# Kernel optimization log

Measured on AMD Instinct MI355X. Metric: run time of the kernel, lower is better.

## Reference

```python
import jax, jax.numpy as jnp
import numpy as np

B, T, R, D = 32, 128, 49, 512
H_EXP, H_CLS = 256, 256
THRES = 0.1
LAM = 4.0
NEG_INF = -1e9


def setup_inputs() -> dict:
    key = jax.random.key(0)
    ks = jax.random.split(key, 16)
    s = 0.02
    return {
        "word_emb": jax.random.normal(ks[0], (B, T, D), jnp.float32),
        "region_emb": jax.random.normal(ks[1], (B, R, D), jnp.float32),
        "attention_mask": jnp.ones((B, T), jnp.int32),
        # pos expert MLP: D -> H_EXP -> 1
        "pw1": jax.random.normal(ks[2], (D, H_EXP), jnp.float32) * s,
        "pb1": jnp.zeros((H_EXP,), jnp.float32),
        "pw2": jax.random.normal(ks[3], (H_EXP, 1), jnp.float32) * s,
        "pb2": jnp.zeros((1,), jnp.float32),
        # neg expert MLP: D -> H_EXP -> 1
        "nw1": jax.random.normal(ks[4], (D, H_EXP), jnp.float32) * s,
        "nb1": jnp.zeros((H_EXP,), jnp.float32),
        "nw2": jax.random.normal(ks[5], (H_EXP, 1), jnp.float32) * s,
        "nb2": jnp.zeros((1,), jnp.float32),
        # fc: D -> 1
        "fcw": jax.random.normal(ks[6], (D, 1), jnp.float32) * s,
        "fcb": jnp.zeros((1,), jnp.float32),
        # classifier: D -> H_CLS -> 2 (dropout is eval-mode identity)
        "cw1": jax.random.normal(ks[7], (D, H_CLS), jnp.float32) * s,
        "cb1": jnp.zeros((H_CLS,), jnp.float32),
        "cw2": jax.random.normal(ks[8], (H_CLS, 2), jnp.float32) * s,
        "cb2": jnp.zeros((2,), jnp.float32),
    }


def _mlp_score(x, w1, b1, w2, b2):
    # sigmoid(Linear(tanh(Linear(x)))) -> squeeze last dim
    return jax.nn.sigmoid(jnp.tanh(x @ w1 + b1) @ w2 + b2)[..., 0]


def reference(word_emb, region_emb, attention_mask,
              pw1, pb1, pw2, pb2, nw1, nb1, nw2, nb2,
              fcw, fcb, cw1, cb1, cw2, cb2):
    mask_f = attention_mask.astype(word_emb.dtype)  # [B,T]

    # cross attention word x region: [B,T,R]
    attn = jnp.einsum("btd,brd->btr", word_emb, region_emb)
    attn_neg = (attn - THRES > 0).astype(attn.dtype)  # [B,T,R]
    attn_pos = jax.nn.softmax(
        jnp.where(attn_neg > 0, attn, NEG_INF) * LAM, axis=-1)
    pos = jnp.einsum("btr,brd->btd", attn_pos, region_emb) + word_emb

    # pos expert: sigmoid score, zeroed where token has no positive region
    # or is padding (padding tokens were excluded by the ragged gather).
    expert_neg_mask = attn_neg.sum(-1) == 0  # [B,T] bool
    pos_score = _mlp_score(pos, pw1, pb1, pw2, pb2)  # [B,T]
    pos_score = jnp.where(expert_neg_mask, 0.0, pos_score) * mask_f
    pos_score = jax.nn.relu(pos_score)
    pos_agg = jnp.einsum("bt,btd->bd", pos_score, pos)

    # neg expert over all (token, region) pair embeddings, masked to the
    # ragged set neg_mask = (1 - attn_neg) * attention_mask
    all_emb = word_emb[:, :, None, :] + region_emb[:, None, :, :]  # [B,T,R,D]
    neg_mask = (1.0 - attn_neg) * mask_f[:, :, None]  # [B,T,R]
    neg_score = _mlp_score(all_emb, nw1, nb1, nw2, nb2)  # [B,T,R]
    neg_score = jax.nn.relu(neg_score * neg_mask)
    neg_agg = jnp.einsum("btr,btrd->bd", neg_score, all_emb)

    result = jnp.stack([neg_agg, pos_agg], axis=1)  # [B,2,D]

    choose = (result @ fcw + fcb)[..., 0]  # [B,2]
    choose_mask = attn_neg.sum(axis=(-1, -2)) == 0  # [B]
    choose = choose.at[:, 0].set(
        jnp.where(choose_mask, NEG_INF, choose[:, 0]))
    path_prob = jax.nn.softmax(choose, axis=-1)  # [B,2]
    final = jnp.einsum("bk,bkd->bd", path_prob, result)  # [B,D]

    logits = jax.nn.relu(final @ cw1 + cb1) @ cw2 + cb2  # [B,2]
    return (logits, path_prob)
```

## Files before the change

kernel.cpp:

```cpp
#include <hip/hip_runtime.h>

#define B_ 32
#define T_ 128
#define R_ 49
#define D_ 512
#define HE_ 256
#define HC_ 256

#define NG_PACK 64
#define NG_K1 512
#define NG_G1 354
#define NG_G2 256
#define NG_NEGB 512

typedef float f32x4 __attribute__((ext_vector_type(4)));
typedef short s16x8 __attribute__((ext_vector_type(8)));
typedef short s16x4 __attribute__((ext_vector_type(4)));

__device__ __forceinline__ unsigned short bf16rne(float f) {
  unsigned u = __float_as_uint(f);
  u += 0x7FFF + ((u >> 16) & 1);
  return (unsigned short)(u >> 16);
}
__device__ __forceinline__ float rcp_fast(float x) {
  return __builtin_amdgcn_rcpf(x);
}
__device__ __forceinline__ float tanh_fast(float x) {
  float e = __expf(2.0f * x);
  return fmaf(-2.0f, rcp_fast(e + 1.0f), 1.0f);
}
__device__ __forceinline__ float sigmoid_fast(float x) {
  return rcp_fast(1.0f + __expf(-x));
}
__device__ __forceinline__ float wave_sum(float v) {
#pragma unroll
  for (int off = 32; off; off >>= 1) v += __shfl_down(v, off);
  return v;
}

__global__ __launch_bounds__(512, 8) void k1_pack(
    const float* __restrict__ word, const float* __restrict__ region,
    const float* __restrict__ nw1, const float* __restrict__ pw1,
    const int* __restrict__ amask, unsigned short* __restrict__ wp,
    float* __restrict__ nsr, float* __restrict__ pos,
    float* __restrict__ negcnt, unsigned long long* __restrict__ nmask) {
  __shared__ float attn_s[8][52];
  __shared__ alignas(16) float wp_T[49][8];
  int tid = threadIdx.x, wave = tid >> 6, lane = tid & 63;
  int bid = blockIdx.x;

  if (bid < NG_PACK) {
    int gid = bid * 512 + tid;
    if (gid < B_ * R_) nsr[gid] = 0.f;
    int mat = gid >> 14;
    int rem = gid & 16383;
    int plane = rem & 63;
    int tile = rem >> 6;
    int kt = tile >> 4, ct = tile & 15;
    const float* W = mat ? pw1 : nw1;
    int k0 = kt * 32 + (plane >> 4) * 8;
    int c = ct * 16 + (plane & 15);
    s16x8 pk;
#pragma unroll
    for (int j = 0; j < 8; ++j)
      pk[j] = (short)bf16rne(W[(size_t)(k0 + j) * HE_ + c]);
    *(s16x8*)(wp + (size_t)gid * 8) = pk;
    return;
  }

  int bid2 = bid - NG_PACK;
  int b = bid2 >> 4;
  int t0 = (bid2 & 15) * 8;
  int bt0 = b * T_ + t0;
  const float* reg = region + (size_t)b * R_ * D_;
  const float4* word4 = (const float4*)word;

#pragma unroll
  for (int pass = 0; pass < 2; ++pass) {
    int tp = pass * 4;
    float4 wv[4][2];
#pragma unroll
    for (int t = 0; t < 4; ++t)
#pragma unroll
      for (int j = 0; j < 2; ++j)
        wv[t][j] = word4[(size_t)(bt0 + tp + t) * 128 + lane * 2 + j];
    for (int r = wave; r < R_; r += 8) {
      const float4* rrow4 = (const float4*)(reg + (size_t)r * D_);
      float4 rv0 = rrow4[lane * 2 + 0];
      float4 rv1 = rrow4[lane * 2 + 1];
#pragma unroll
      for (int t = 0; t < 4; ++t) {
        float4 w0 = wv[t][0], w1 = wv[t][1];
        float acc = 0.f;
        acc = fmaf(w0.x, rv0.x, acc);
        acc = fmaf(w0.y, rv0.y, acc);
        acc = fmaf(w0.z, rv0.z, acc);
        acc = fmaf(w0.w, rv0.w, acc);
        acc = fmaf(w1.x, rv1.x, acc);
        acc = fmaf(w1.y, rv1.y, acc);
        acc = fmaf(w1.z, rv1.z, acc);
        acc = fmaf(w1.w, rv1.w, acc);
        acc = wave_sum(acc);
        if (lane == 0) attn_s[tp + t][r] = acc;
      }
    }
  }
  __syncthreads();

  {
    int t = wave;
    int am = amask[bt0 + t];
    float a = (lane < R_) ? attn_s[t][lane] : 0.f;
    float neg = (lane < R_ && (a - 0.1f) > 0.f) ? 1.f : 0.f;
    float masked = (lane < R_) ? ((neg > 0.f) ? a * 4.0f : -4e9f) : -3.0e38f;
    float cnt = wave_sum(neg);
    float m = masked;
#pragma unroll
    for (int off = 32; off; off >>= 1) m = fmaxf(m, __shfl_down(m, off));
    m = __shfl(m, 0);
    float e = (lane < R_) ? __expf(masked - m) : 0.f;
    float s = wave_sum(e);
    s = __shfl(s, 0);
    if (lane < R_) wp_T[lane][t] = e / s;
    bool want = (lane < R_) && (neg == 0.f) && (am != 0);
    unsigned long long bm = __ballot(want);
    if (lane == 0) {
      negcnt[bt0 + t] = cnt;
      nmask[bt0 + t] = bm;
    }
  }
  __syncthreads();

  int d = tid;
  float accs[8] = {0.f, 0.f, 0.f, 0.f, 0.f, 0.f, 0.f, 0.f};
#pragma unroll 7
  for (int r = 0; r < R_; ++r) {
    float g = reg[(size_t)r * D_ + d];
    float4 w0 = *(const float4*)&wp_T[r][0];
    float4 w1 = *(const float4*)&wp_T[r][4];
    accs[0] = fmaf(w0.x, g, accs[0]);
    accs[1] = fmaf(w0.y, g, accs[1]);
    accs[2] = fmaf(w0.z, g, accs[2]);
    accs[3] = fmaf(w0.w, g, accs[3]);
    accs[4] = fmaf(w1.x, g, accs[4]);
    accs[5] = fmaf(w1.y, g, accs[5]);
    accs[6] = fmaf(w1.z, g, accs[6]);
    accs[7] = fmaf(w1.w, g, accs[7]);
  }
#pragma unroll
  for (int t = 0; t < 8; ++t) {
    size_t base = (size_t)(bt0 + t) * D_ + d;
    pos[base] = word[base] + accs[t];
  }
}

__global__ __launch_bounds__(512) void gemm_all(
    const float* __restrict__ word, const float* __restrict__ region,
    const float* __restrict__ pos, const unsigned short* __restrict__ wpack,
    const float* __restrict__ nb1, const float* __restrict__ pb1,
    const float* __restrict__ pw2, const float* __restrict__ pb2,
    const float* __restrict__ negcnt, const int* __restrict__ amask,
    float* __restrict__ wh, float* __restrict__ rh,
    float* __restrict__ pscore) {
  __shared__ alignas(16) unsigned short As[16 * 512];
  __shared__ float sred[16][4];
  int tid = threadIdx.x, wave = tid >> 6, lane = tid & 63;
  int bid = blockIdx.x;

  bool isg2 = (bid >= NG_G1);
  const float* A;
  float* outp = nullptr;
  int row0;
  bool useb = false;
  const s16x8* Wp8;
  if (!isg2) {
    if (bid < 256) {
      A = word; outp = wh; row0 = bid * 16; useb = true;
    } else {
      A = region; outp = rh; row0 = (bid - 256) * 16;
    }
    Wp8 = (const s16x8*)wpack;
  } else {
    A = pos; row0 = (bid - NG_G1) * 16;
    Wp8 = (const s16x8*)wpack + 16384;
  }
  const float4* A4 = (const float4*)(A + (size_t)row0 * D_);
#pragma unroll
  for (int it = 0; it < 4; ++it) {
    int f = it * 512 + tid;
    int row = f >> 7, kq = f & 127;
    float4 v = A4[f];
    int bo = (row * 1024 + kq * 8) ^ ((row & 7) << 4);
    s16x4 pk;
    pk[0] = (short)bf16rne(v.x);
    pk[1] = (short)bf16rne(v.y);
    pk[2] = (short)bf16rne(v.z);
    pk[3] = (short)bf16rne(v.w);
    *(s16x4*)((char*)As + bo) = pk;
  }
  __syncthreads();
  int rl = lane & 15, kg = lane >> 4;
  f32x4 acc0 = {0.f, 0.f, 0.f, 0.f}, acc1 = {0.f, 0.f, 0.f, 0.f};
  int ct0 = wave, ct1 = wave + 8;
#pragma unroll
  for (int kt = 0; kt < 16; ++kt) {
    int bo = (rl * 1024 + kt * 64 + kg * 16) ^ ((rl & 7) << 4);
    s16x8 af = *(const s16x8*)((char*)As + bo);
    s16x8 b0 = Wp8[(size_t)(kt * 16 + ct0) * 64 + lane];
    s16x8 b1 = Wp8[(size_t)(kt * 16 + ct1) * 64 + lane];
    acc0 = __builtin_amdgcn_mfma_f32_16x16x32_bf16(af, b0, acc0, 0, 0, 0);
    acc1 = __builtin_amdgcn_mfma_f32_16x16x32_bf16(af, b1, acc1, 0, 0, 0);
  }
  if (!isg2) {
    float bb0 = useb ? nb1[ct0 * 16 + rl] : 0.f;
    float bb1 = useb ? nb1[ct1 * 16 + rl] : 0.f;
    int r0 = row0 + kg * 4;
#pragma unroll
    for (int q = 0; q < 4; ++q) {
      outp[(size_t)(r0 + q) * HE_ + ct0 * 16 + rl] = acc0[q] + bb0;
      outp[(size_t)(r0 + q) * HE_ + ct1 * 16 + rl] = acc1[q] + bb1;
    }
    return;
  }
  __syncthreads();
  float* hp_s = (float*)As;
#pragma unroll
  for (int q = 0; q < 4; ++q) {
    hp_s[(kg * 4 + q) * 256 + ct0 * 16 + rl] = acc0[q];
    hp_s[(kg * 4 + q) * 256 + ct1 * 16 + rl] = acc1[q];
  }
  __syncthreads();
  int c = tid & 255, jh = tid >> 8;
  float pb1c = pb1[c], pw2c = pw2[c];
#pragma unroll
  for (int jj = 0; jj < 8; ++jj) {
    int j = jh * 8 + jj;
    float v = tanh_fast(hp_s[j * 256 + c] + pb1c) * pw2c;
    v = wave_sum(v);
    if (lane == 0) sred[j][wave & 3] = v;
  }
  __syncthreads();
  if (tid < 16) {
    float s = sred[tid][0] + sred[tid][1] + sred[tid][2] + sred[tid][3] +
              pb2[0];
    s = sigmoid_fast(s);
    int row = row0 + tid;
    if (negcnt[row] == 0.f) s = 0.f;
    s *= (float)amask[row];
    pscore[row] = fmaxf(s, 0.f);
  }
}

__global__ __launch_bounds__(512, 6) void neg_expert(
    const float* __restrict__ wh, const float* __restrict__ rh,
    const float* __restrict__ nw2, const float* __restrict__ nb2,
    const unsigned long long* __restrict__ nmask, float* __restrict__ nst,
    float* __restrict__ nsr) {
  __shared__ alignas(16) float rh_s[R_ * HE_];
  __shared__ int plist[400];
  __shared__ float nst_l[8];
  __shared__ float nsr_l[52];
  __shared__ int cnt_s[8];
  __shared__ int off_s[8];
  __shared__ int P_s;
  int tid = threadIdx.x, wave = tid >> 6, lane = tid & 63;
  int nb = blockIdx.x;
  int b = nb >> 4, t0 = (nb & 15) * 8;
  int bt0 = b * T_ + t0;
  {
    const float4* src = (const float4*)(rh + (size_t)b * R_ * HE_);
    float4* dst = (float4*)rh_s;
    for (int i = tid; i < R_ * (HE_ / 4); i += 512) dst[i] = src[i];
  }
  if (tid < 8) {
    nst_l[tid] = 0.f;
    cnt_s[tid] = __popcll(nmask[bt0 + tid]);
  }
  if (tid < R_) nsr_l[tid] = 0.f;
  __syncthreads();
  if (tid == 0) {
    int tot = 0;
#pragma unroll
    for (int w = 0; w < 8; ++w) {
      off_s[w] = tot;
      tot += cnt_s[w];
    }
    P_s = tot;
  }
  __syncthreads();
  {
    unsigned long long mw = nmask[bt0 + wave];
    if (lane < R_ && ((mw >> lane) & 1ull)) {
      int pfx = __popcll(mw & ((1ull << lane) - 1ull));
      plist[off_s[wave] + pfx] = (wave << 6) | lane;
    }
  }
  __syncthreads();
  int P = P_s;
  int grp = tid >> 4, gl = tid & 15;
  float4 wnr[4];
#pragma unroll
  for (int k = 0; k < 4; ++k)
    wnr[k] = ((const float4*)nw2)[4 * gl + ((gl + k) & 3)];
  float bias = nb2[0];
  for (int i = grp; i < P; i += 32) {
    int tr = plist[i];
    int t = tr >> 6, r = tr & 63;
    const float4* wrow = (const float4*)(wh + (size_t)(bt0 + t) * HE_);
    const float4* rrow = (const float4*)(rh_s + r * HE_);
    float acc = 0.f;
#pragma unroll
    for (int k = 0; k < 4; ++k) {
      int c = 4 * gl + ((gl + k) & 3);
      float4 hw = wrow[c];
      float4 hr = rrow[c];
      float4 wn = wnr[k];
      acc = fmaf(tanh_fast(hw.x + hr.x), wn.x, acc);
      acc = fmaf(tanh_fast(hw.y + hr.y), wn.y, acc);
      acc = fmaf(tanh_fast(hw.z + hr.z), wn.z, acc);
      acc = fmaf(tanh_fast(hw.w + hr.w), wn.w, acc);
    }
    acc += __shfl_xor(acc, 1);
    acc += __shfl_xor(acc, 2);
    acc += __shfl_xor(acc, 4);
    acc += __shfl_xor(acc, 8);
    if (gl == 0) {
      float s = sigmoid_fast(acc + bias);
      atomicAdd(&nst_l[t], s);
      atomicAdd(&nsr_l[r], s);
    }
  }
  __syncthreads();
  if (tid < 8) {
    nst[bt0 + tid] = nst_l[tid];
  } else if (tid >= 64 && tid < 64 + R_) {
    atomicAdd(&nsr[b * R_ + (tid - 64)], nsr_l[tid - 64]);
  }
}

__global__ __launch_bounds__(512) void k7a_agg(
    const float* __restrict__ word, const float* __restrict__ region,
    const float* __restrict__ pos, const float* __restrict__ pscore,
    const float* __restrict__ nst, const float* __restrict__ nsr,
    float* __restrict__ nagg, float* __restrict__ pagg) {
  int b = blockIdx.x >> 3, dc = blockIdx.x & 7;
  int tid = threadIdx.x;
  int dl = tid & 63, ts = tid >> 6;
  int d = dc * 64 + dl;
  __shared__ float nst_s[T_], psc_s[T_], nsr_s[R_];
  __shared__ float redn[8][64], redp[8][64];
  if (tid < T_) {
    psc_s[tid] = pscore[b * T_ + tid];
    nst_s[tid] = nst[b * T_ + tid];
  } else if (tid < T_ + R_) {
    nsr_s[tid - T_] = nsr[b * R_ + (tid - T_)];
  }
  __syncthreads();
  float na = 0.f, pa = 0.f;
  for (int t = ts; t < T_; t += 8) {
    size_t base = ((size_t)(b * T_ + t)) * D_ + d;
    na = fmaf(nst_s[t], word[base], na);
    pa = fmaf(psc_s[t], pos[base], pa);
  }
  for (int r = ts; r < R_; r += 8)
    na = fmaf(nsr_s[r], region[((size_t)(b * R_ + r)) * D_ + d], na);
  redn[ts][dl] = na;
  redp[ts][dl] = pa;
  __syncthreads();
  if (tid < 64) {
    float s = 0.f;
#pragma unroll
    for (int k = 0; k < 8; ++k) s += redn[k][tid];
    nagg[(size_t)b * D_ + dc * 64 + tid] = s;
  } else if (tid < 128) {
    int l = tid - 64;
    float s = 0.f;
#pragma unroll
    for (int k = 0; k < 8; ++k) s += redp[k][l];
    pagg[(size_t)b * D_ + dc * 64 + l] = s;
  }
}

__global__ __launch_bounds__(256) void k7b_tail(
    const float* __restrict__ nagg, const float* __restrict__ pagg,
    const float* __restrict__ negcnt, const float* __restrict__ fcw,
    const float* __restrict__ fcb, const float* __restrict__ cw1,
    const float* __restrict__ cb1, const float* __restrict__ cw2,
    const float* __restrict__ cb2, float* __restrict__ out) {
  int b = blockIdx.x, tid = threadIdx.x, lane = tid & 63, wave = tid >> 6;
  __shared__ float na_s[D_], pa_s[D_], fin[D_];
  __shared__ float red[8];
  __shared__ float pp0, pp1;
  float cntp = (tid < T_) ? negcnt[b * T_ + tid] : 0.f;
  float cw = wave_sum(cntp);
  if (lane == 0) red[wave] = cw;
  int d0 = tid, d1 = tid + 256;
  float n0 = nagg[(size_t)b * D_ + d0], n1 = nagg[(size_t)b * D_ + d1];
  float p0 = pagg[(size_t)b * D_ + d0], p1 = pagg[(size_t)b * D_ + d1];
  na_s[d0] = n0;
  na_s[d1] = n1;
  pa_s[d0] = p0;
  pa_s[d1] = p1;
  __syncthreads();
  float cnt_total = red[0] + red[1] + red[2] + red[3];
  float f0 = fcw[d0], f1 = fcw[d1];
  float c0p = n0 * f0 + n1 * f1;
  float c1p = p0 * f0 + p1 * f1;
  c0p = wave_sum(c0p);
  c1p = wave_sum(c1p);
  __syncthreads();
  if (lane == 0) { red[wave] = c0p; red[wave + 4] = c1p; }
  __syncthreads();
  if (tid == 0) {
    float c0 = red[0] + red[1] + red[2] + red[3] + fcb[0];
    float c1 = red[4] + red[5] + red[6] + red[7] + fcb[0];
    if (cnt_total == 0.f) c0 = -1e9f;
    float m = fmaxf(c0, c1);
    float e0 = __expf(c0 - m), e1 = __expf(c1 - m);
    float inv = 1.f / (e0 + e1);
    pp0 = e0 * inv;
    pp1 = e1 * inv;
    out[2 * B_ + 2 * b + 0] = pp0;
    out[2 * B_ + 2 * b + 1] = pp1;
  }
  __syncthreads();
  for (int d = tid; d < D_; d += 256) fin[d] = pp0 * na_s[d] + pp1 * pa_s[d];
  __syncthreads();
  float a0 = cb1[tid], a1 = 0.f, a2 = 0.f, a3 = 0.f;
#pragma unroll 4
  for (int d = 0; d < D_; d += 4) {
    a0 = fmaf(fin[d + 0], cw1[(size_t)(d + 0) * HC_ + tid], a0);
    a1 = fmaf(fin[d + 1], cw1[(size_t)(d + 1) * HC_ + tid], a1);
    a2 = fmaf(fin[d + 2], cw1[(size_t)(d + 2) * HC_ + tid], a2);
    a3 = fmaf(fin[d + 3], cw1[(size_t)(d + 3) * HC_ + tid], a3);
  }
  float acc = fmaxf((a0 + a1) + (a2 + a3), 0.f);
  float l0 = acc * cw2[2 * tid + 0];
  float l1 = acc * cw2[2 * tid + 1];
  l0 = wave_sum(l0);
  l1 = wave_sum(l1);
  __syncthreads();
  if (lane == 0) { red[wave] = l0; red[wave + 4] = l1; }
  __syncthreads();
  if (tid == 0) {
    out[2 * b + 0] = red[0] + red[1] + red[2] + red[3] + cb2[0];
    out[2 * b + 1] = red[4] + red[5] + red[6] + red[7] + cb2[1];
  }
}

extern "C" void kernel_launch(void* const* d_in, const int* in_sizes, int n_in,
                              void* d_out, int out_size, void* d_ws,
                              size_t ws_size, hipStream_t stream) {
  const float* word = (const float*)d_in[0];
  const float* region = (const float*)d_in[1];
  const int* amask = (const int*)d_in[2];
  const float* pw1 = (const float*)d_in[3];
  const float* pb1 = (const float*)d_in[4];
  const float* pw2 = (const float*)d_in[5];
  const float* pb2 = (const float*)d_in[6];
  const float* nw1 = (const float*)d_in[7];
  const float* nb1 = (const float*)d_in[8];
  const float* nw2 = (const float*)d_in[9];
  const float* nb2 = (const float*)d_in[10];
  const float* fcw = (const float*)d_in[11];
  const float* fcb = (const float*)d_in[12];
  const float* cw1 = (const float*)d_in[13];
  const float* cb1 = (const float*)d_in[14];
  const float* cw2 = (const float*)d_in[15];
  const float* cb2 = (const float*)d_in[16];
  float* out = (float*)d_out;

  unsigned short* wpack = (unsigned short*)d_ws;
  float* ws = (float*)d_ws + 131072;
  float* pos = ws;
  float* wh = pos + (size_t)B_ * T_ * D_;
  float* rh = wh + (size_t)B_ * T_ * HE_;
  float* nst = rh + (size_t)B_ * R_ * HE_;
  float* nsr = nst + (size_t)B_ * T_;
  float* negcnt = nsr + (size_t)B_ * R_;
  float* pscore = negcnt + B_ * T_;
  float* nagg = pscore + B_ * T_;
  float* pagg = nagg + (size_t)B_ * D_;
  unsigned long long* nmask =
      (unsigned long long*)(pagg + (size_t)B_ * D_);

  k1_pack<<<NG_PACK + NG_K1, 512, 0, stream>>>(
      word, region, nw1, pw1, amask, wpack, nsr, pos, negcnt, nmask);
  gemm_all<<<NG_G1 + NG_G2, 512, 0, stream>>>(
      word, region, pos, wpack, nb1, pb1, pw2, pb2, negcnt, amask, wh, rh,
      pscore);
  neg_expert<<<NG_NEGB, 512, 0, stream>>>(wh, rh, nw2, nb2, nmask, nst, nsr);
  k7a_agg<<<B_ * 8, 512, 0, stream>>>(word, region, pos, pscore, nst, nsr,
                                      nagg, pagg);
  k7b_tail<<<B_, 256, 0, stream>>>(nagg, pagg, negcnt, fcw, fcb, cw1, cb1,
                                   cw2, cb2, out);
}
```

Measured before the change: 85.13 us.

## Enlarge GEMM row tiles, restructure attention dot, replace nsr atomics with slices

The GEMM kernel now handles 32 rows per block instead of 16, reusing each loaded weight fragment across two MFMA sub-tiles and halving the grid. The word-region attention dot in k1 is restructured so each 16-lane group handles one token, replacing full-wave reductions with 16-lane xor shuffles and cutting per-region reductions. The global atomicAdd on nsr is replaced by per-block slice writes summed in k7a, which also removes the zero-initialisation in k1. The k1 launch bound is relaxed to allow more registers. Together these target reduction overhead, weight reloads and atomic contention, at the cost of more LDS per GEMM block and fewer blocks in flight.

Result: faster. 75.96 us (-10.8%).

```diff
diff --git a/kernel.cpp b/kernel.cpp
--- a/kernel.cpp
+++ b/kernel.cpp
@@ -9,8 +9,8 @@
 
 #define NG_PACK 64
 #define NG_K1 512
-#define NG_G1 354
-#define NG_G2 256
+#define NG_G1 177
+#define NG_G2 128
 #define NG_NEGB 512
 
 typedef float f32x4 __attribute__((ext_vector_type(4)));
@@ -38,12 +38,12 @@
   return v;
 }
 
-__global__ __launch_bounds__(512, 8) void k1_pack(
+__global__ __launch_bounds__(512, 4) void k1_pack(
     const float* __restrict__ word, const float* __restrict__ region,
     const float* __restrict__ nw1, const float* __restrict__ pw1,
     const int* __restrict__ amask, unsigned short* __restrict__ wp,
-    float* __restrict__ nsr, float* __restrict__ pos,
-    float* __restrict__ negcnt, unsigned long long* __restrict__ nmask) {
+    float* __restrict__ pos, float* __restrict__ negcnt,
+    unsigned long long* __restrict__ nmask) {
   __shared__ float attn_s[8][52];
   __shared__ alignas(16) float wp_T[49][8];
   int tid = threadIdx.x, wave = tid >> 6, lane = tid & 63;
@@ -51,7 +51,6 @@
 
   if (bid < NG_PACK) {
     int gid = bid * 512 + tid;
-    if (gid < B_ * R_) nsr[gid] = 0.f;
     int mat = gid >> 14;
     int rem = gid & 16383;
     int plane = rem & 63;
@@ -74,35 +73,36 @@
   int bt0 = b * T_ + t0;
   const float* reg = region + (size_t)b * R_ * D_;
   const float4* word4 = (const float4*)word;
-
-#pragma unroll
-  for (int pass = 0; pass < 2; ++pass) {
-    int tp = pass * 4;
-    float4 wv[4][2];
-#pragma unroll
-    for (int t = 0; t < 4; ++t)
-#pragma unroll
-      for (int j = 0; j < 2; ++j)
-        wv[t][j] = word4[(size_t)(bt0 + tp + t) * 128 + lane * 2 + j];
-    for (int r = wave; r < R_; r += 8) {
-      const float4* rrow4 = (const float4*)(reg + (size_t)r * D_);
-      float4 rv0 = rrow4[lane * 2 + 0];
-      float4 rv1 = rrow4[lane * 2 + 1];
-#pragma unroll
-      for (int t = 0; t < 4; ++t) {
-        float4 w0 = wv[t][0], w1 = wv[t][1];
-        float acc = 0.f;
-        acc = fmaf(w0.x, rv0.x, acc);
-        acc = fmaf(w0.y, rv0.y, acc);
-        acc = fmaf(w0.z, rv0.z, acc);
-        acc = fmaf(w0.w, rv0.w, acc);
-        acc = fmaf(w1.x, rv1.x, acc);
-        acc = fmaf(w1.y, rv1.y, acc);
-        acc = fmaf(w1.z, rv1.z, acc);
-        acc = fmaf(w1.w, rv1.w, acc);
-        acc = wave_sum(acc);
-        if (lane == 0) attn_s[tp + t][r] = acc;
+  int il = lane & 15, g = lane >> 4;
+
+  float4 wv[2][8];
+#pragma unroll
+  for (int q = 0; q < 2; ++q)
+#pragma unroll
+    for (int kq = 0; kq < 8; ++kq)
+      wv[q][kq] = word4[(size_t)(bt0 + q * 4 + g) * 128 + il + kq * 16];
+
+  for (int r = wave; r < R_; r += 8) {
+    const float4* rrow4 = (const float4*)(reg + (size_t)r * D_);
+    float4 rv[8];
+#pragma unroll
+    for (int kq = 0; kq < 8; ++kq) rv[kq] = rrow4[il + kq * 16];
+#pragma unroll
+    for (int q = 0; q < 2; ++q) {
+      float acc = 0.f;
+#pragma unroll
+      for (int kq = 0; kq < 8; ++kq) {
+        float4 w = wv[q][kq], rr = rv[kq];
+        acc = fmaf(w.x, rr.x, acc);
+        acc = fmaf(w.y, rr.y, acc);
+        acc = fmaf(w.z, rr.z, acc);
+        acc = fmaf(w.w, rr.w, acc);
       }
+      acc += __shfl_xor(acc, 8);
+      acc += __shfl_xor(acc, 4);
+      acc += __shfl_xor(acc, 2);
+      acc += __shfl_xor(acc, 1);
+      if (il == 0) attn_s[q * 4 + g][r] = acc;
     }
   }
   __syncthreads();
@@ -135,17 +135,17 @@
   float accs[8] = {0.f, 0.f, 0.f, 0.f, 0.f, 0.f, 0.f, 0.f};
 #pragma unroll 7
   for (int r = 0; r < R_; ++r) {
-    float g = reg[(size_t)r * D_ + d];
+    float gg = reg[(size_t)r * D_ + d];
     float4 w0 = *(const float4*)&wp_T[r][0];
     float4 w1 = *(const float4*)&wp_T[r][4];
-    accs[0] = fmaf(w0.x, g, accs[0]);
-    accs[1] = fmaf(w0.y, g, accs[1]);
-    accs[2] = fmaf(w0.z, g, accs[2]);
-    accs[3] = fmaf(w0.w, g, accs[3]);
-    accs[4] = fmaf(w1.x, g, accs[4]);
-    accs[5] = fmaf(w1.y, g, accs[5]);
-    accs[6] = fmaf(w1.z, g, accs[6]);
-    accs[7] = fmaf(w1.w, g, accs[7]);
+    accs[0] = fmaf(w0.x, gg, accs[0]);
+    accs[1] = fmaf(w0.y, gg, accs[1]);
+    accs[2] = fmaf(w0.z, gg, accs[2]);
+    accs[3] = fmaf(w0.w, gg, accs[3]);
+    accs[4] = fmaf(w1.x, gg, accs[4]);
+    accs[5] = fmaf(w1.y, gg, accs[5]);
+    accs[6] = fmaf(w1.z, gg, accs[6]);
+    accs[7] = fmaf(w1.w, gg, accs[7]);
   }
 #pragma unroll
   for (int t = 0; t < 8; ++t) {
@@ -162,8 +162,8 @@
     const float* __restrict__ negcnt, const int* __restrict__ amask,
     float* __restrict__ wh, float* __restrict__ rh,
     float* __restrict__ pscore) {
-  __shared__ alignas(16) unsigned short As[16 * 512];
-  __shared__ float sred[16][4];
+  __shared__ alignas(16) unsigned short As[32 * 512];
+  __shared__ float sred[32][4];
   int tid = threadIdx.x, wave = tid >> 6, lane = tid & 63;
   int bid = blockIdx.x;
 
@@ -174,19 +174,19 @@
   bool useb = false;
   const s16x8* Wp8;
   if (!isg2) {
-    if (bid < 256) {
-      A = word; outp = wh; row0 = bid * 16; useb = true;
+    if (bid < 128) {
+      A = word; outp = wh; row0 = bid * 32; useb = true;
     } else {
-      A = region; outp = rh; row0 = (bid - 256) * 16;
+      A = region; outp = rh; row0 = (bid - 128) * 32;
     }
     Wp8 = (const s16x8*)wpack;
   } else {
-    A = pos; row0 = (bid - NG_G1) * 16;
+    A = pos; row0 = (bid - NG_G1) * 32;
     Wp8 = (const s16x8*)wpack + 16384;
   }
   const float4* A4 = (const float4*)(A + (size_t)row0 * D_);
 #pragma unroll
-  for (int it = 0; it < 4; ++it) {
+  for (int it = 0; it < 8; ++it) {
     int f = it * 512 + tid;
     int row = f >> 7, kq = f & 127;
     float4 v = A4[f];
@@ -200,47 +200,59 @@
   }
   __syncthreads();
   int rl = lane & 15, kg = lane >> 4;
-  f32x4 acc0 = {0.f, 0.f, 0.f, 0.f}, acc1 = {0.f, 0.f, 0.f, 0.f};
   int ct0 = wave, ct1 = wave + 8;
+  f32x4 acc[2][2];
+#pragma unroll
+  for (int s = 0; s < 2; ++s)
+#pragma unroll
+    for (int ci = 0; ci < 2; ++ci) acc[s][ci] = (f32x4){0.f, 0.f, 0.f, 0.f};
 #pragma unroll
   for (int kt = 0; kt < 16; ++kt) {
-    int bo = (rl * 1024 + kt * 64 + kg * 16) ^ ((rl & 7) << 4);
-    s16x8 af = *(const s16x8*)((char*)As + bo);
     s16x8 b0 = Wp8[(size_t)(kt * 16 + ct0) * 64 + lane];
     s16x8 b1 = Wp8[(size_t)(kt * 16 + ct1) * 64 + lane];
-    acc0 = __builtin_amdgcn_mfma_f32_16x16x32_bf16(af, b0, acc0, 0, 0, 0);
-    acc1 = __builtin_amdgcn_mfma_f32_16x16x32_bf16(af, b1, acc1, 0, 0, 0);
+#pragma unroll
+    for (int sub = 0; sub < 2; ++sub) {
+      int bo = ((sub * 16 + rl) * 1024 + kt * 64 + kg * 16) ^ ((rl & 7) << 4);
+      s16x8 af = *(const s16x8*)((char*)As + bo);
+      acc[sub][0] = __builtin_amdgcn_mfma_f32_16x16x32_bf16(af, b0, acc[sub][0], 0, 0, 0);
+      acc[sub][1] = __builtin_amdgcn_mfma_f32_16x16x32_bf16(af, b1, acc[sub][1], 0, 0, 0);
+    }
   }
   if (!isg2) {
     float bb0 = useb ? nb1[ct0 * 16 + rl] : 0.f;
     float bb1 = useb ? nb1[ct1 * 16 + rl] : 0.f;
-    int r0 = row0 + kg * 4;
+#pragma unroll
+    for (int sub = 0; sub < 2; ++sub) {
+      int r0 = row0 + sub * 16 + kg * 4;
+#pragma unroll
+      for (int q = 0; q < 4; ++q) {
+        outp[(size_t)(r0 + q) * HE_ + ct0 * 16 + rl] = acc[sub][0][q] + bb0;
+        outp[(size_t)(r0 + q) * HE_ + ct1 * 16 + rl] = acc[sub][1][q] + bb1;
+      }
+    }
+    return;
+  }
+  __syncthreads();
+  float* hp_s = (float*)As;
+#pragma unroll
+  for (int sub = 0; sub < 2; ++sub)
 #pragma unroll
     for (int q = 0; q < 4; ++q) {
-      outp[(size_t)(r0 + q) * HE_ + ct0 * 16 + rl] = acc0[q] + bb0;
-      outp[(size_t)(r0 + q) * HE_ + ct1 * 16 + rl] = acc1[q] + bb1;
-    }
-    return;
-  }
-  __syncthreads();
-  float* hp_s = (float*)As;
-#pragma unroll
-  for (int q = 0; q < 4; ++q) {
-    hp_s[(kg * 4 + q) * 256 + ct0 * 16 + rl] = acc0[q];
-    hp_s[(kg * 4 + q) * 256 + ct1 * 16 + rl] = acc1[q];
-  }
+      hp_s[(sub * 16 + kg * 4 + q) * 256 + ct0 * 16 + rl] = acc[sub][0][q];
+      hp_s[(sub * 16 + kg * 4 + q) * 256 + ct1 * 16 + rl] = acc[sub][1][q];
+    }
   __syncthreads();
   int c = tid & 255, jh = tid >> 8;
   float pb1c = pb1[c], pw2c = pw2[c];
 #pragma unroll
-  for (int jj = 0; jj < 8; ++jj) {
-    int j = jh * 8 + jj;
+  for (int jj = 0; jj < 16; ++jj) {
+    int j = jh * 16 + jj;
     float v = tanh_fast(hp_s[j * 256 + c] + pb1c) * pw2c;
     v = wave_sum(v);
     if (lane == 0) sred[j][wave & 3] = v;
   }
   __syncthreads();
-  if (tid < 16) {
+  if (tid < 32) {
     float s = sred[tid][0] + sred[tid][1] + sred[tid][2] + sred[tid][3] +
               pb2[0];
     s = sigmoid_fast(s);
@@ -255,7 +267,7 @@
     const float* __restrict__ wh, const float* __restrict__ rh,
     const float* __restrict__ nw2, const float* __restrict__ nb2,
     const unsigned long long* __restrict__ nmask, float* __restrict__ nst,
-    float* __restrict__ nsr) {
+    float* __restrict__ nsr_sl) {
   __shared__ alignas(16) float rh_s[R_ * HE_];
   __shared__ int plist[400];
   __shared__ float nst_l[8];
@@ -334,14 +346,14 @@
   if (tid < 8) {
     nst[bt0 + tid] = nst_l[tid];
   } else if (tid >= 64 && tid < 64 + R_) {
-    atomicAdd(&nsr[b * R_ + (tid - 64)], nsr_l[tid - 64]);
+    nsr_sl[(size_t)nb * R_ + (tid - 64)] = nsr_l[tid - 64];
   }
 }
 
 __global__ __launch_bounds__(512) void k7a_agg(
     const float* __restrict__ word, const float* __restrict__ region,
     const float* __restrict__ pos, const float* __restrict__ pscore,
-    const float* __restrict__ nst, const float* __restrict__ nsr,
+    const float* __restrict__ nst, const float* __restrict__ nsr_sl,
     float* __restrict__ nagg, float* __restrict__ pagg) {
   int b = blockIdx.x >> 3, dc = blockIdx.x & 7;
   int tid = threadIdx.x;
@@ -353,7 +365,12 @@
     psc_s[tid] = pscore[b * T_ + tid];
     nst_s[tid] = nst[b * T_ + tid];
   } else if (tid < T_ + R_) {
-    nsr_s[tid - T_] = nsr[b * R_ + (tid - T_)];
+    int r = tid - T_;
+    float s = 0.f;
+#pragma unroll
+    for (int tt = 0; tt < 16; ++tt)
+      s += nsr_sl[(size_t)(b * 16 + tt) * R_ + r];
+    nsr_s[r] = s;
   }
   __syncthreads();
   float na = 0.f, pa = 0.f;
@@ -476,8 +493,8 @@
   float* wh = pos + (size_t)B_ * T_ * D_;
   float* rh = wh + (size_t)B_ * T_ * HE_;
   float* nst = rh + (size_t)B_ * R_ * HE_;
-  float* nsr = nst + (size_t)B_ * T_;
-  float* negcnt = nsr + (size_t)B_ * R_;
+  float* nsr_sl = nst + (size_t)B_ * T_;
+  float* negcnt = nsr_sl + (size_t)B_ * 16 * R_;
   float* pscore = negcnt + B_ * T_;
   float* nagg = pscore + B_ * T_;
   float* pagg = nagg + (size_t)B_ * D_;
@@ -485,12 +502,13 @@
       (unsigned long long*)(pagg + (size_t)B_ * D_);
 
   k1_pack<<<NG_PACK + NG_K1, 512, 0, stream>>>(
-      word, region, nw1, pw1, amask, wpack, nsr, pos, negcnt, nmask);
+      word, region, nw1, pw1, amask, wpack, pos, negcnt, nmask);
   gemm_all<<<NG_G1 + NG_G2, 512, 0, stream>>>(
       word, region, pos, wpack, nb1, pb1, pw2, pb2, negcnt, amask, wh, rh,
       pscore);
-  neg_expert<<<NG_NEGB, 512, 0, stream>>>(wh, rh, nw2, nb2, nmask, nst, nsr);
-  k7a_agg<<<B_ * 8, 512, 0, stream>>>(word, region, pos, pscore, nst, nsr,
+  neg_expert<<<NG_NEGB, 512, 0, stream>>>(wh, rh, nw2, nb2, nmask, nst,
+                                          nsr_sl);
+  k7a_agg<<<B_ * 8, 512, 0, stream>>>(word, region, pos, pscore, nst, nsr_sl,
                                       nagg, pagg);
   k7b_tail<<<B_, 256, 0, stream>>>(nagg, pagg, negcnt, fcw, fcb, cw1, cb1,
                                    cw2, cb2, out);
```
